# Performance work log

Hardware: AMD Instinct MI355X
Metric: run time of the kernel (lower is better)

The kernel has to match this reference:

```python
import jax, jax.numpy as jnp
import numpy as np

BETA = 0.25  # commitment cost from cfg.beta


def setup_inputs() -> dict:
    key = jax.random.key(0)
    k1, k2 = jax.random.split(key)
    z = jax.random.normal(k1, (32, 256, 32, 32), dtype=jnp.float32)
    # codebook initialized uniform(-1/D, 1/D) as in the torch module
    D = 256
    embedding = jax.random.uniform(k2, (1024, D), dtype=jnp.float32,
                                   minval=-1.0 / D, maxval=1.0 / D)
    return {"z": z, "embedding": embedding}


def reference(z, embedding):
    b, c, h, w = z.shape
    # (B,C,H,W) -> (B*H*W, C)
    z_flat = jnp.transpose(z, (0, 2, 3, 1)).reshape(-1, c)
    # squared euclidean distances: ||z||^2 - 2 z.E^T + ||e||^2  -> [N, K]
    d = (jnp.sum(z_flat * z_flat, axis=1, keepdims=True)
         - 2.0 * z_flat @ embedding.T
         + jnp.sum(embedding * embedding, axis=1)[None, :])
    idx = jnp.argmin(d, axis=1)                       # [N]
    z_q_flat = embedding[idx]                         # [N, C]
    z_q = jnp.transpose(z_q_flat.reshape(b, h, w, c), (0, 3, 1, 2))
    # straight-through estimator
    z_q_st = z + jax.lax.stop_gradient(z_q - z)
    codebook_loss = jnp.mean((z_q - jax.lax.stop_gradient(z)) ** 2)
    commitment_loss = jnp.mean((z - jax.lax.stop_gradient(z_q)) ** 2)
    vq_loss = codebook_loss + BETA * commitment_loss
    return z_q_st, vq_loss, idx.reshape(b, h, w)
```

## Files before the change

### kernel.cpp

```cpp
#include <hip/hip_runtime.h>


#define TAU 4.0e-4f

typedef __attribute__((ext_vector_type(8))) short short8b;
typedef __attribute__((ext_vector_type(4))) float f32x4;

__device__ __forceinline__ unsigned short f2bf_rne(float x) {
  unsigned int u = __float_as_uint(x);
  unsigned int r = u + 0x7fffu + ((u >> 16) & 1u);
  return (unsigned short)(r >> 16);
}
__device__ __forceinline__ float bf2f(unsigned short s) {
  return __uint_as_float(((unsigned int)s) << 16);
}

__device__ __forceinline__ float np_pairwise256_sq(const float* a) {
  float tot = 0.0f;
#pragma unroll
  for (int blk = 0; blk < 2; ++blk) {
    const float* p = a + blk * 128;
    float r[8];
#pragma unroll
    for (int j = 0; j < 8; ++j) r[j] = __fmul_rn(p[j], p[j]);
    for (int i = 8; i < 128; i += 8) {
#pragma unroll
      for (int j = 0; j < 8; ++j) r[j] = __fadd_rn(r[j], __fmul_rn(p[i + j], p[i + j]));
    }
    float res = __fadd_rn(__fadd_rn(__fadd_rn(r[0], r[1]), __fadd_rn(r[2], r[3])),
                          __fadd_rn(__fadd_rn(r[4], r[5]), __fadd_rn(r[6], r[7])));
    tot = (blk == 0) ? res : __fadd_rn(tot, res);
  }
  return tot;
}

__global__ __launch_bounds__(256) void enormK(const float* __restrict__ emb,
                                              float* __restrict__ enorm) {
  const int k = blockIdx.x * 256 + threadIdx.x;
  enorm[k] = np_pairwise256_sq(emb + (size_t)k * 256);
}

__global__ __launch_bounds__(256) void transK(const float* __restrict__ emb,
                                              float* __restrict__ eT) {
  __shared__ float t[32][33];
  const int k0 = blockIdx.x * 32, d0 = blockIdx.y * 32;
  const int lx = threadIdx.x & 31, ly = threadIdx.x >> 5;
#pragma unroll
  for (int r = 0; r < 4; ++r)
    t[ly + r * 8][lx] = emb[(size_t)(k0 + ly + r * 8) * 256 + d0 + lx];
  __syncthreads();
#pragma unroll
  for (int r = 0; r < 4; ++r)
    eT[(size_t)(d0 + ly + r * 8) * 1024 + k0 + lx] = t[lx][ly + r * 8];
}

__global__ __launch_bounds__(256) void prepBK(const float* __restrict__ emb,
                                              unsigned short* __restrict__ bp,
                                              double* loss_sum, int* rcount) {
  const int C = blockIdx.x;
  const int t = threadIdx.x;
  if (C == 0 && t == 0) { *loss_sum = 0.0; *rcount = 0; }
  const int n = t & 15, kb = (t >> 4) & 7, limb = t >> 7;
  const float* er = emb + (size_t)(C * 16 + n) * 256 + kb * 32;
#pragma unroll
  for (int s = 0; s < 4; ++s) {
    unsigned int w[4];
#pragma unroll
    for (int p = 0; p < 4; ++p) {
      unsigned short v2[2];
#pragma unroll
      for (int q = 0; q < 2; ++q) {
        float x = er[s * 8 + p * 2 + q];
        unsigned short hi = f2bf_rne(x);
        v2[q] = (limb == 0) ? hi : f2bf_rne(x - bf2f(hi));
      }
      w[p] = (unsigned int)v2[0] | ((unsigned int)v2[1] << 16);
    }
    size_t idx = ((size_t)(C * 16 + limb * 8 + kb) * 64 + (n + 16 * s)) * 8;
    *(uint4*)(bp + idx) = make_uint4(w[0], w[1], w[2], w[3]);
  }
}

__global__ __launch_bounds__(256) void distK(const float* __restrict__ z,
                                             const unsigned short* __restrict__ bp,
                                             const float* __restrict__ enorm,
                                             int* __restrict__ idx_buf,
                                             float* __restrict__ out,
                                             int* __restrict__ rlist,
                                             int* __restrict__ rcount) {
  const int tid = threadIdx.x;
  const int wid = tid >> 6, lane = tid & 63;
  const int R = blockIdx.x * 4 + wid;
  const int n0w = R * 16;
  const int b = n0w >> 10, hw0 = n0w & 1023;
  const int s = lane >> 4, m = lane & 15;
  const float* zb = z + (size_t)b * 262144 + hw0 + m;

  short8b az[8], al[8];
#pragma unroll
  for (int kb = 0; kb < 8; ++kb) {
    float f[8];
#pragma unroll
    for (int i = 0; i < 8; ++i)
      f[i] = zb[(size_t)(kb * 32 + s * 8 + i) * 1024];
#pragma unroll
    for (int i = 0; i < 8; ++i) {
      unsigned short hi = f2bf_rne(f[i]);
      az[kb][i] = (short)hi;
      al[kb][i] = (short)f2bf_rne(f[i] - bf2f(hi));
    }
  }

  float m1[4], m2[4];
  int k1i[4];
#pragma unroll
  for (int r = 0; r < 4; ++r) { m1[r] = 3.0e38f; m2[r] = 3.0e38f; k1i[r] = 0; }

  short8b be[8], bl[8];
#pragma unroll
  for (int kb = 0; kb < 8; ++kb)
    be[kb] = *(const short8b*)(bp + ((size_t)kb * 64 + lane) * 8);

  for (int nt = 0; nt < 64; ++nt) {
    f32x4 acc = {0.0f, 0.0f, 0.0f, 0.0f};
    float en = enorm[nt * 16 + m];
#pragma unroll
    for (int kb = 0; kb < 8; ++kb)
      acc = __builtin_amdgcn_mfma_f32_16x16x32_bf16(az[kb], be[kb], acc, 0, 0, 0);
#pragma unroll
    for (int kb = 0; kb < 8; ++kb)
      bl[kb] = *(const short8b*)(bp + ((size_t)(nt * 16 + 8 + kb) * 64 + lane) * 8);
#pragma unroll
    for (int kb = 0; kb < 8; ++kb)
      acc = __builtin_amdgcn_mfma_f32_16x16x32_bf16(al[kb], be[kb], acc, 0, 0, 0);
    if (nt < 63) {
#pragma unroll
      for (int kb = 0; kb < 8; ++kb)
        be[kb] = *(const short8b*)(bp + ((size_t)((nt + 1) * 16 + kb) * 64 + lane) * 8);
    }
#pragma unroll
    for (int kb = 0; kb < 8; ++kb)
      acc = __builtin_amdgcn_mfma_f32_16x16x32_bf16(az[kb], bl[kb], acc, 0, 0, 0);
    const int code = nt * 16 + m;
#pragma unroll
    for (int r = 0; r < 4; ++r) {
      float v = en - 2.0f * acc[r];
      if (v < m1[r]) { m2[r] = m1[r]; m1[r] = v; k1i[r] = code; }
      else if (v < m2[r]) { m2[r] = v; }
    }
  }

#pragma unroll
  for (int r = 0; r < 4; ++r) {
    float a1 = m1[r], a2 = m2[r];
    int ai = k1i[r];
#pragma unroll
    for (int mask = 1; mask < 16; mask <<= 1) {
      float b1 = __shfl_xor(a1, mask);
      float b2 = __shfl_xor(a2, mask);
      int bi = __shfl_xor(ai, mask);
      if (b1 < a1 || (b1 == a1 && bi < ai)) { a2 = fminf(a1, b2); a1 = b1; ai = bi; }
      else { a2 = fminf(a2, b1); }
    }
    if (m == 0) {
      int n = n0w + s * 4 + r;
      idx_buf[n] = ai;
      out[(size_t)8388609 + n] = (float)ai;
      if (a2 - a1 < TAU) {
        int p = atomicAdd(rcount, 1);
        rlist[p] = n;
      }
    }
  }
}

__global__ __launch_bounds__(64) void refineK(const float* __restrict__ z,
                                              const float* __restrict__ eT,
                                              const float* __restrict__ enorm,
                                              const int* __restrict__ rlist,
                                              const int* __restrict__ rcount,
                                              int* __restrict__ idx_buf,
                                              float* __restrict__ out) {
  __shared__ float zw[256];
  const int lane = threadIdx.x;
  const int cnt = *rcount;
  for (int ii = blockIdx.x; ii < cnt; ii += gridDim.x) {
    const int n = rlist[ii];
    const int bb = n >> 10, hw = n & 1023;
#pragma unroll
    for (int s = 0; s < 4; ++s)
      zw[lane + s * 64] = z[(size_t)bb * 262144 + (size_t)(lane + s * 64) * 1024 + hw];
    const float a32 = np_pairwise256_sq(zw);

    float bch[16];
#pragma unroll
    for (int j = 0; j < 16; ++j) bch[j] = 0.0f;
    const float* eb = eT + lane * 16;

    float4 B0[4], B1[4], B2[4], B3[4];
#pragma unroll
    for (int q = 0; q < 4; ++q) {
      B0[q] = *(const float4*)(eb + (size_t)0 * 1024 + q * 4);
      B1[q] = *(const float4*)(eb + (size_t)1 * 1024 + q * 4);
      B2[q] = *(const float4*)(eb + (size_t)2 * 1024 + q * 4);
      B3[q] = *(const float4*)(eb + (size_t)3 * 1024 + q * 4);
    }
#pragma unroll 1
    for (int d = 0; d < 256; d += 4) {
      const bool more = (d + 4) < 256;
      {
        float zv = zw[d];
#pragma unroll
        for (int q = 0; q < 4; ++q) {
          bch[q * 4 + 0] = __fmaf_rn(zv, B0[q].x, bch[q * 4 + 0]);
          bch[q * 4 + 1] = __fmaf_rn(zv, B0[q].y, bch[q * 4 + 1]);
          bch[q * 4 + 2] = __fmaf_rn(zv, B0[q].z, bch[q * 4 + 2]);
          bch[q * 4 + 3] = __fmaf_rn(zv, B0[q].w, bch[q * 4 + 3]);
        }
        if (more) {
#pragma unroll
          for (int q = 0; q < 4; ++q)
            B0[q] = *(const float4*)(eb + (size_t)(d + 4) * 1024 + q * 4);
        }
      }
      {
        float zv = zw[d + 1];
#pragma unroll
        for (int q = 0; q < 4; ++q) {
          bch[q * 4 + 0] = __fmaf_rn(zv, B1[q].x, bch[q * 4 + 0]);
          bch[q * 4 + 1] = __fmaf_rn(zv, B1[q].y, bch[q * 4 + 1]);
          bch[q * 4 + 2] = __fmaf_rn(zv, B1[q].z, bch[q * 4 + 2]);
          bch[q * 4 + 3] = __fmaf_rn(zv, B1[q].w, bch[q * 4 + 3]);
        }
        if (more) {
#pragma unroll
          for (int q = 0; q < 4; ++q)
            B1[q] = *(const float4*)(eb + (size_t)(d + 5) * 1024 + q * 4);
        }
      }
      {
        float zv = zw[d + 2];
#pragma unroll
        for (int q = 0; q < 4; ++q) {
          bch[q * 4 + 0] = __fmaf_rn(zv, B2[q].x, bch[q * 4 + 0]);
          bch[q * 4 + 1] = __fmaf_rn(zv, B2[q].y, bch[q * 4 + 1]);
          bch[q * 4 + 2] = __fmaf_rn(zv, B2[q].z, bch[q * 4 + 2]);
          bch[q * 4 + 3] = __fmaf_rn(zv, B2[q].w, bch[q * 4 + 3]);
        }
        if (more) {
#pragma unroll
          for (int q = 0; q < 4; ++q)
            B2[q] = *(const float4*)(eb + (size_t)(d + 6) * 1024 + q * 4);
        }
      }
      {
        float zv = zw[d + 3];
#pragma unroll
        for (int q = 0; q < 4; ++q) {
          bch[q * 4 + 0] = __fmaf_rn(zv, B3[q].x, bch[q * 4 + 0]);
          bch[q * 4 + 1] = __fmaf_rn(zv, B3[q].y, bch[q * 4 + 1]);
          bch[q * 4 + 2] = __fmaf_rn(zv, B3[q].z, bch[q * 4 + 2]);
          bch[q * 4 + 3] = __fmaf_rn(zv, B3[q].w, bch[q * 4 + 3]);
        }
        if (more) {
#pragma unroll
          for (int q = 0; q < 4; ++q)
            B3[q] = *(const float4*)(eb + (size_t)(d + 7) * 1024 + q * 4);
        }
      }
    }

    float best = 3.0e38f;
    int bi = 1 << 30;
#pragma unroll
    for (int j = 0; j < 16; ++j) {
      const int k = lane * 16 + j;
      float tb = __fmul_rn(2.0f, bch[j]);
      float d32 = __fadd_rn(__fsub_rn(a32, tb), enorm[k]);
      if (d32 < best) { best = d32; bi = k; }
    }
#pragma unroll
    for (int mask = 1; mask < 64; mask <<= 1) {
      float ov = __shfl_xor(best, mask);
      int oi = __shfl_xor(bi, mask);
      if (ov < best || (ov == best && oi < bi)) { best = ov; bi = oi; }
    }
    if (lane == 0) {
      idx_buf[n] = bi;
      out[(size_t)8388609 + n] = (float)bi;
    }
  }
}

__global__ __launch_bounds__(256) void outputK(const float* __restrict__ z,
                                               const float* __restrict__ emb,
                                               const int* __restrict__ idx_buf,
                                               float* __restrict__ out,
                                               double* __restrict__ loss_sum) {
  __shared__ float el[64 * 65];
  __shared__ int sidx[64];
  __shared__ double sloss[4];

  const int tid = threadIdx.x;
  const int rg = blockIdx.x >> 2;
  const int q = blockIdx.x & 3;
  const int n0 = rg * 64;
  const int b = n0 >> 10;
  const int hw0 = n0 & 1023;

  if (tid < 64) sidx[tid] = idx_buf[n0 + tid];
  __syncthreads();

#pragma unroll
  for (int rep = 0; rep < 16; ++rep) {
    int idx = rep * 256 + tid;
    int r = idx >> 6, i = idx & 63;
    el[r * 65 + i] = emb[(size_t)sidx[r] * 256 + q * 64 + i];
  }
  __syncthreads();

  const int mq = (tid & 15) * 4;
  const int cg = tid >> 4;
  const size_t zb = (size_t)b * 262144 + hw0 + mq;
  double acc = 0.0;
#pragma unroll
  for (int it = 0; it < 4; ++it) {
    int cl = it * 16 + cg;
    int c = q * 64 + cl;
    float4 z4 = *(const float4*)(z + zb + (size_t)c * 1024);
    float e0 = el[(mq + 0) * 65 + cl];
    float e1 = el[(mq + 1) * 65 + cl];
    float e2 = el[(mq + 2) * 65 + cl];
    float e3 = el[(mq + 3) * 65 + cl];
    float d0 = e0 - z4.x, d1 = e1 - z4.y, d2 = e2 - z4.z, d3 = e3 - z4.w;
    float4 o = make_float4(z4.x + d0, z4.y + d1, z4.z + d2, z4.w + d3);
    *(float4*)(out + zb + (size_t)c * 1024) = o;
    acc += (double)(d0 * d0) + (double)(d1 * d1) +
           (double)(d2 * d2) + (double)(d3 * d3);
  }
  for (int mask = 1; mask < 64; mask <<= 1) acc += __shfl_xor(acc, mask);
  if ((tid & 63) == 0) sloss[tid >> 6] = acc;
  __syncthreads();
  if (tid == 0)
    atomicAdd(loss_sum, sloss[0] + sloss[1] + sloss[2] + sloss[3]);
}

__global__ void finalK(const double* loss_sum, float* out) {
  double s = *loss_sum;
  out[8388608] = (float)(1.25 * s / 8388608.0);
}

extern "C" void kernel_launch(void* const* d_in, const int* in_sizes, int n_in,
                              void* d_out, int out_size, void* d_ws, size_t ws_size,
                              hipStream_t stream) {
  const float* z = (const float*)d_in[0];
  const float* emb = (const float*)d_in[1];
  float* out = (float*)d_out;
  char* ws = (char*)d_ws;
  double* loss_sum = (double*)ws;
  int* rcount = (int*)(ws + 16);
  float* enorm = (float*)(ws + 64);
  unsigned short* bp = (unsigned short*)(ws + 4352);
  float* eT = (float*)(ws + 1052928);
  int* idx_buf = (int*)(ws + 2494720);
  int* rlist = (int*)(ws + 2625792);

  enormK<<<4, 256, 0, stream>>>(emb, enorm);
  transK<<<dim3(32, 8), 256, 0, stream>>>(emb, eT);
  prepBK<<<64, 256, 0, stream>>>(emb, bp, loss_sum, rcount);
  distK<<<512, 256, 0, stream>>>(z, bp, enorm, idx_buf, out, rlist, rcount);
  refineK<<<2048, 64, 0, stream>>>(z, eT, enorm, rlist, rcount, idx_buf, out);
  outputK<<<2048, 256, 0, stream>>>(z, emb, idx_buf, out, loss_sum);
  finalK<<<1, 1, 0, stream>>>(loss_sum, out);
}
```

Before: 194.0 us.

## Drop codebook low limb in distance MFMA, merge prep kernels, fuse final loss

The codebook is now packed as a single bf16 limb, so the distance loop issues two MFMA groups per tile (z hi and z lo against the codebook) instead of three, and prefetches only the next tile's codebook fragments. To absorb the extra error, the refinement threshold TAU is raised so more rows are sent to the exact fp32 refine pass. The three prep kernels are merged into one launch. The final loss kernel is replaced by a last-block-done atomic counter in outputK. This removes a third of the matrix work and two launches, at the cost of more rows needing refinement.

After: 266.2 us. +37.2%, slower.

```diff
diff --git a/kernel.cpp b/kernel.cpp
--- a/kernel.cpp
+++ b/kernel.cpp
@@ -1,7 +1,7 @@
 #include <hip/hip_runtime.h>
 
 
-#define TAU 4.0e-4f
+#define TAU 1.0e-3f
 
 typedef __attribute__((ext_vector_type(8))) short short8b;
 typedef __attribute__((ext_vector_type(4))) float f32x4;
@@ -34,50 +34,48 @@
   return tot;
 }
 
-__global__ __launch_bounds__(256) void enormK(const float* __restrict__ emb,
-                                              float* __restrict__ enorm) {
-  const int k = blockIdx.x * 256 + threadIdx.x;
-  enorm[k] = np_pairwise256_sq(emb + (size_t)k * 256);
-}
-
-__global__ __launch_bounds__(256) void transK(const float* __restrict__ emb,
-                                              float* __restrict__ eT) {
-  __shared__ float t[32][33];
-  const int k0 = blockIdx.x * 32, d0 = blockIdx.y * 32;
-  const int lx = threadIdx.x & 31, ly = threadIdx.x >> 5;
-#pragma unroll
-  for (int r = 0; r < 4; ++r)
-    t[ly + r * 8][lx] = emb[(size_t)(k0 + ly + r * 8) * 256 + d0 + lx];
-  __syncthreads();
-#pragma unroll
-  for (int r = 0; r < 4; ++r)
-    eT[(size_t)(d0 + ly + r * 8) * 1024 + k0 + lx] = t[lx][ly + r * 8];
-}
-
-__global__ __launch_bounds__(256) void prepBK(const float* __restrict__ emb,
-                                              unsigned short* __restrict__ bp,
-                                              double* loss_sum, int* rcount) {
-  const int C = blockIdx.x;
+__global__ __launch_bounds__(256) void prepK(const float* __restrict__ emb,
+                                             float* __restrict__ enorm,
+                                             float* __restrict__ eT,
+                                             unsigned short* __restrict__ bp,
+                                             double* loss_sum, int* rcount,
+                                             int* done) {
+  __shared__ float tt[32][33];
+  const int blk = blockIdx.x;
   const int t = threadIdx.x;
-  if (C == 0 && t == 0) { *loss_sum = 0.0; *rcount = 0; }
-  const int n = t & 15, kb = (t >> 4) & 7, limb = t >> 7;
-  const float* er = emb + (size_t)(C * 16 + n) * 256 + kb * 32;
-#pragma unroll
-  for (int s = 0; s < 4; ++s) {
-    unsigned int w[4];
-#pragma unroll
-    for (int p = 0; p < 4; ++p) {
-      unsigned short v2[2];
-#pragma unroll
-      for (int q = 0; q < 2; ++q) {
-        float x = er[s * 8 + p * 2 + q];
-        unsigned short hi = f2bf_rne(x);
-        v2[q] = (limb == 0) ? hi : f2bf_rne(x - bf2f(hi));
-      }
-      w[p] = (unsigned int)v2[0] | ((unsigned int)v2[1] << 16);
-    }
-    size_t idx = ((size_t)(C * 16 + limb * 8 + kb) * 64 + (n + 16 * s)) * 8;
-    *(uint4*)(bp + idx) = make_uint4(w[0], w[1], w[2], w[3]);
+  if (blk == 0 && t == 0) { *loss_sum = 0.0; *rcount = 0; *done = 0; }
+  if (blk < 4) {
+    const int k = blk * 256 + t;
+    enorm[k] = np_pairwise256_sq(emb + (size_t)k * 256);
+  } else if (blk < 260) {
+    const int local = blk - 4;
+    const int k0 = (local & 31) * 32, d0 = (local >> 5) * 32;
+    const int lx = t & 31, ly = t >> 5;
+#pragma unroll
+    for (int r = 0; r < 4; ++r)
+      tt[ly + r * 8][lx] = emb[(size_t)(k0 + ly + r * 8) * 256 + d0 + lx];
+    __syncthreads();
+#pragma unroll
+    for (int r = 0; r < 4; ++r)
+      eT[(size_t)(d0 + ly + r * 8) * 1024 + k0 + lx] = tt[lx][ly + r * 8];
+  } else {
+    const int C = blk - 260;
+    const int n = t & 15, kb = (t >> 4) & 7, half = t >> 7;
+    const float* er = emb + (size_t)(C * 16 + n) * 256 + kb * 32;
+#pragma unroll
+    for (int ss = 0; ss < 2; ++ss) {
+      const int s = half * 2 + ss;
+      unsigned int w[4];
+#pragma unroll
+      for (int p = 0; p < 4; ++p) {
+        unsigned short v2[2];
+#pragma unroll
+        for (int q = 0; q < 2; ++q) v2[q] = f2bf_rne(er[s * 8 + p * 2 + q]);
+        w[p] = (unsigned int)v2[0] | ((unsigned int)v2[1] << 16);
+      }
+      size_t idx = ((size_t)(C * 8 + kb) * 64 + (n + 16 * s)) * 8;
+      *(uint4*)(bp + idx) = make_uint4(w[0], w[1], w[2], w[3]);
+    }
   }
 }
 
@@ -116,7 +114,7 @@
 #pragma unroll
   for (int r = 0; r < 4; ++r) { m1[r] = 3.0e38f; m2[r] = 3.0e38f; k1i[r] = 0; }
 
-  short8b be[8], bl[8];
+  short8b be[8], bn[8];
 #pragma unroll
   for (int kb = 0; kb < 8; ++kb)
     be[kb] = *(const short8b*)(bp + ((size_t)kb * 64 + lane) * 8);
@@ -127,20 +125,15 @@
 #pragma unroll
     for (int kb = 0; kb < 8; ++kb)
       acc = __builtin_amdgcn_mfma_f32_16x16x32_bf16(az[kb], be[kb], acc, 0, 0, 0);
+    const int ntn = (nt < 63) ? nt + 1 : 0;
 #pragma unroll
     for (int kb = 0; kb < 8; ++kb)
-      bl[kb] = *(const short8b*)(bp + ((size_t)(nt * 16 + 8 + kb) * 64 + lane) * 8);
+      bn[kb] = *(const short8b*)(bp + (((size_t)ntn * 8 + kb) * 64 + lane) * 8);
 #pragma unroll
     for (int kb = 0; kb < 8; ++kb)
       acc = __builtin_amdgcn_mfma_f32_16x16x32_bf16(al[kb], be[kb], acc, 0, 0, 0);
-    if (nt < 63) {
-#pragma unroll
-      for (int kb = 0; kb < 8; ++kb)
-        be[kb] = *(const short8b*)(bp + ((size_t)((nt + 1) * 16 + kb) * 64 + lane) * 8);
-    }
-#pragma unroll
-    for (int kb = 0; kb < 8; ++kb)
-      acc = __builtin_amdgcn_mfma_f32_16x16x32_bf16(az[kb], bl[kb], acc, 0, 0, 0);
+#pragma unroll
+    for (int kb = 0; kb < 8; ++kb) be[kb] = bn[kb];
     const int code = nt * 16 + m;
 #pragma unroll
     for (int r = 0; r < 4; ++r) {
@@ -296,7 +289,8 @@
                                                const float* __restrict__ emb,
                                                const int* __restrict__ idx_buf,
                                                float* __restrict__ out,
-                                               double* __restrict__ loss_sum) {
+                                               double* __restrict__ loss_sum,
+                                               int* __restrict__ done) {
   __shared__ float el[64 * 65];
   __shared__ int sidx[64];
   __shared__ double sloss[4];
@@ -341,13 +335,15 @@
   for (int mask = 1; mask < 64; mask <<= 1) acc += __shfl_xor(acc, mask);
   if ((tid & 63) == 0) sloss[tid >> 6] = acc;
   __syncthreads();
-  if (tid == 0)
+  if (tid == 0) {
     atomicAdd(loss_sum, sloss[0] + sloss[1] + sloss[2] + sloss[3]);
-}
-
-__global__ void finalK(const double* loss_sum, float* out) {
-  double s = *loss_sum;
-  out[8388608] = (float)(1.25 * s / 8388608.0);
+    __threadfence();
+    unsigned int old = atomicAdd((unsigned int*)done, 1u);
+    if (old == (unsigned int)(gridDim.x - 1)) {
+      double sum = atomicAdd(loss_sum, 0.0);
+      out[8388608] = (float)(1.25 * sum / 8388608.0);
+    }
+  }
 }
 
 extern "C" void kernel_launch(void* const* d_in, const int* in_sizes, int n_in,
@@ -359,17 +355,15 @@
   char* ws = (char*)d_ws;
   double* loss_sum = (double*)ws;
   int* rcount = (int*)(ws + 16);
+  int* done = (int*)(ws + 32);
   float* enorm = (float*)(ws + 64);
   unsigned short* bp = (unsigned short*)(ws + 4352);
   float* eT = (float*)(ws + 1052928);
   int* idx_buf = (int*)(ws + 2494720);
   int* rlist = (int*)(ws + 2625792);
 
-  enormK<<<4, 256, 0, stream>>>(emb, enorm);
-  transK<<<dim3(32, 8), 256, 0, stream>>>(emb, eT);
-  prepBK<<<64, 256, 0, stream>>>(emb, bp, loss_sum, rcount);
+  prepK<<<324, 256, 0, stream>>>(emb, enorm, eT, bp, loss_sum, rcount, done);
   distK<<<512, 256, 0, stream>>>(z, bp, enorm, idx_buf, out, rlist, rcount);
   refineK<<<2048, 64, 0, stream>>>(z, eT, enorm, rlist, rcount, idx_buf, out);
-  outputK<<<2048, 256, 0, stream>>>(z, emb, idx_buf, out, loss_sum);
-  finalK<<<1, 1, 0, stream>>>(loss_sum, out);
-}
+  outputK<<<2048, 256, 0, stream>>>(z, emb, idx_buf, out, loss_sum, done);
+}
```
